# Kernel optimization log

Measured on AMD Instinct MI355X. Metric: run time of the kernel, lower is better.

The kernel has to match this reference:

```python
import jax, jax.numpy as jnp
import numpy as np

S, A, B, D = 4, 64, 2048, 384
H1, H2, H3 = 128, 128, 64


def setup_inputs() -> dict:
    key = jax.random.key(0)
    ks = jax.random.split(key, 6)
    x = jax.random.normal(ks[0], (B, A, D), dtype=jnp.float32)
    species = jax.random.randint(ks[1], (A,), 0, S, dtype=jnp.int32)
    # per-species stacked MLP weights, scaled ~1/sqrt(fan_in) like reset_parameters
    W0 = jax.random.normal(ks[2], (S, D, H1), dtype=jnp.float32) / np.sqrt(D)
    W1 = jax.random.normal(ks[3], (S, H1, H2), dtype=jnp.float32) / np.sqrt(H1)
    W2 = jax.random.normal(ks[4], (S, H2, H3), dtype=jnp.float32) / np.sqrt(H2)
    W3 = jax.random.normal(ks[5], (S, H3, 1), dtype=jnp.float32) / np.sqrt(H3)
    b0 = jnp.zeros((S, H1), jnp.float32)
    b1 = jnp.zeros((S, H2), jnp.float32)
    b2 = jnp.zeros((S, H3), jnp.float32)
    b3 = jnp.zeros((S, 1), jnp.float32)
    return {"x": x, "species": species, "W0": W0, "b0": b0, "W1": W1,
            "b1": b1, "W2": W2, "b2": b2, "W3": W3, "b3": b3}


def reference(x, species, W0, b0, W1, b1, W2, b2, W3, b3):
    # Gather per-atom species weights once, then batched per-atom GEMMs.
    # x: [B, A, D]; species: [A]
    y = jnp.einsum('bad,adh->bah', x, W0[species]) + b0[species]
    y = jnp.exp(-y * y)
    y = jnp.einsum('bah,ahk->bak', y, W1[species]) + b1[species]
    y = jnp.exp(-y * y)
    y = jnp.einsum('bak,akm->bam', y, W2[species]) + b2[species]
    y = jnp.exp(-y * y)
    y = jnp.einsum('bam,amo->bao', y, W3[species]) + b3[species]  # [B, A, 1]
    return jnp.squeeze(jnp.sum(y, axis=1))  # [B]
```

## Files before the change

kernel.cpp:

```cpp
#include <hip/hip_runtime.h>

#define S_DIM 4
#define A_DIM 64
#define B_DIM 2048
#define D_DIM 384
#define H1D 128
#define H2D 128
#define H3D 64
#define MT 64

typedef __attribute__((ext_vector_type(8))) short short8;
typedef __attribute__((ext_vector_type(4))) float float4v;

__device__ __forceinline__ unsigned short f2bf(float f) {
  unsigned u = __float_as_uint(f);
  u += 0x7FFFu + ((u >> 16) & 1u);
  return (unsigned short)(u >> 16);
}

__device__ __forceinline__ void store_bf4(unsigned short* p, float4v v) {
  union { unsigned short s[4]; uint2 u; } t;
  t.s[0] = f2bf(v[0]); t.s[1] = f2bf(v[1]);
  t.s[2] = f2bf(v[2]); t.s[3] = f2bf(v[3]);
  *(uint2*)p = t.u;
}

__global__ __launch_bounds__(256) void prep_weights(
    const float* __restrict__ W0, const float* __restrict__ W1,
    const float* __restrict__ W2,
    unsigned short* __restrict__ W0T, unsigned short* __restrict__ W1T,
    unsigned short* __restrict__ W2T) {
  __shared__ float tile[32][33];
  int b = blockIdx.x;
  const float* src; unsigned short* dst; int R, C, dt, ht, s;
  if (b < 192) {
    s = b / 48; int t = b % 48; dt = t / 4; ht = t % 4;
    src = W0 + s * D_DIM * H1D; dst = W0T + s * H1D * D_DIM; R = D_DIM; C = H1D;
  } else if (b < 256) {
    int bb = b - 192; s = bb / 16; int t = bb % 16; dt = t / 4; ht = t % 4;
    src = W1 + s * H1D * H2D; dst = W1T + s * H2D * H1D; R = H1D; C = H2D;
  } else {
    int bb = b - 256; s = bb / 8; int t = bb % 8; dt = t / 2; ht = t % 2;
    src = W2 + s * H2D * H3D; dst = W2T + s * H3D * H2D; R = H2D; C = H3D;
  }
  int tx = threadIdx.x & 31, ty = threadIdx.x >> 5;
#pragma unroll
  for (int k = 0; k < 4; ++k)
    tile[ty + 8 * k][tx] = src[(size_t)(dt * 32 + ty + 8 * k) * C + ht * 32 + tx];
  __syncthreads();
#pragma unroll
  for (int k = 0; k < 4; ++k)
    dst[(size_t)(ht * 32 + ty + 8 * k) * R + dt * 32 + tx] = f2bf(tile[tx][ty + 8 * k]);
}

__global__ __launch_bounds__(256, 4) void mlp_fused(
    const float* __restrict__ x, const int* __restrict__ species,
    const unsigned short* __restrict__ W0T, const unsigned short* __restrict__ W1T,
    const unsigned short* __restrict__ W2T,
    const float* __restrict__ b0, const float* __restrict__ b1,
    const float* __restrict__ b2, const float* __restrict__ W3,
    const float* __restrict__ b3, float* __restrict__ out) {
  __shared__ __align__(16) unsigned short xbuf0[MT * 136];
  __shared__ __align__(16) unsigned short xbuf1[MT * 136];
  __shared__ float W3s[H3D];
  unsigned short* H0 = xbuf1;
  unsigned short* H1 = xbuf0;
  float* H2 = (float*)xbuf1;

  const int a = blockIdx.y;
  const int brow0 = blockIdx.x * MT;
  const int sp = species[a];
  const int tid = threadIdx.x;
  const int wave = tid >> 6;
  const int lane = tid & 63;
  const int q = lane >> 4;
  const int r = lane & 15;

  const float4v zero = {0.f, 0.f, 0.f, 0.f};

  const int srow = tid >> 2;
  const int c4 = tid & 3;
  const float* xrow = x + ((size_t)(brow0 + srow) * A_DIM + a) * D_DIM + c4 * 4;
  const unsigned short* w0base =
      W0T + (size_t)sp * H1D * D_DIM + (wave * 32 + r) * D_DIM + q * 8;

  float4v xv[8];
#pragma unroll
  for (int j = 0; j < 8; ++j) xv[j] = *(const float4v*)(xrow + j * 16);
  if (tid < H3D) W3s[tid] = W3[sp * H3D + tid];
  short8 bf[4][2];
#pragma unroll
  for (int kk = 0; kk < 4; ++kk)
#pragma unroll
    for (int n = 0; n < 2; ++n)
      bf[kk][n] = *(const short8*)(w0base + n * 16 * D_DIM + kk * 32);
  {
    unsigned short* xd = xbuf0 + srow * 136 + c4 * 4;
#pragma unroll
    for (int j = 0; j < 8; ++j) store_bf4(xd + j * 16, xv[j]);
  }
  __syncthreads();

  float4v acc0[4][2];
#pragma unroll
  for (int g = 0; g < 4; ++g) { acc0[g][0] = zero; acc0[g][1] = zero; }

#pragma unroll
  for (int j = 0; j < 8; ++j) xv[j] = *(const float4v*)(xrow + 128 + j * 16);
#pragma unroll
  for (int g = 0; g < 4; ++g)
#pragma unroll
    for (int kk = 0; kk < 4; ++kk) {
      short8 af = *(const short8*)(xbuf0 + (g * 16 + r) * 136 + kk * 32 + q * 8);
      acc0[g][0] = __builtin_amdgcn_mfma_f32_16x16x32_bf16(af, bf[kk][0], acc0[g][0], 0, 0, 0);
      acc0[g][1] = __builtin_amdgcn_mfma_f32_16x16x32_bf16(af, bf[kk][1], acc0[g][1], 0, 0, 0);
    }
  {
    unsigned short* xd = xbuf1 + srow * 136 + c4 * 4;
#pragma unroll
    for (int j = 0; j < 8; ++j) store_bf4(xd + j * 16, xv[j]);
  }
  __syncthreads();

#pragma unroll
  for (int kk = 0; kk < 4; ++kk)
#pragma unroll
    for (int n = 0; n < 2; ++n)
      bf[kk][n] = *(const short8*)(w0base + n * 16 * D_DIM + 128 + kk * 32);
#pragma unroll
  for (int j = 0; j < 8; ++j) xv[j] = *(const float4v*)(xrow + 256 + j * 16);
#pragma unroll
  for (int g = 0; g < 4; ++g)
#pragma unroll
    for (int kk = 0; kk < 4; ++kk) {
      short8 af = *(const short8*)(xbuf1 + (g * 16 + r) * 136 + kk * 32 + q * 8);
      acc0[g][0] = __builtin_amdgcn_mfma_f32_16x16x32_bf16(af, bf[kk][0], acc0[g][0], 0, 0, 0);
      acc0[g][1] = __builtin_amdgcn_mfma_f32_16x16x32_bf16(af, bf[kk][1], acc0[g][1], 0, 0, 0);
    }
  {
    unsigned short* xd = xbuf0 + srow * 136 + c4 * 4;
#pragma unroll
    for (int j = 0; j < 8; ++j) store_bf4(xd + j * 16, xv[j]);
  }
  __syncthreads();

#pragma unroll
  for (int kk = 0; kk < 4; ++kk)
#pragma unroll
    for (int n = 0; n < 2; ++n)
      bf[kk][n] = *(const short8*)(w0base + n * 16 * D_DIM + 256 + kk * 32);
#pragma unroll
  for (int g = 0; g < 4; ++g)
#pragma unroll
    for (int kk = 0; kk < 4; ++kk) {
      short8 af = *(const short8*)(xbuf0 + (g * 16 + r) * 136 + kk * 32 + q * 8);
      acc0[g][0] = __builtin_amdgcn_mfma_f32_16x16x32_bf16(af, bf[kk][0], acc0[g][0], 0, 0, 0);
      acc0[g][1] = __builtin_amdgcn_mfma_f32_16x16x32_bf16(af, bf[kk][1], acc0[g][1], 0, 0, 0);
    }
  {
    const float* b0p = b0 + sp * H1D;
#pragma unroll
    for (int n = 0; n < 2; ++n) {
      float bias = b0p[wave * 32 + n * 16 + r];
#pragma unroll
      for (int g = 0; g < 4; ++g)
#pragma unroll
        for (int i = 0; i < 4; ++i) {
          float y = acc0[g][n][i] + bias;
          H0[(g * 16 + q * 4 + i) * 136 + wave * 32 + n * 16 + r] = f2bf(__expf(-y * y));
        }
    }
  }
  __syncthreads();

  {
    float4v acc1[4][2];
#pragma unroll
    for (int g = 0; g < 4; ++g) { acc1[g][0] = zero; acc1[g][1] = zero; }
    const unsigned short* w1base =
        W1T + (size_t)sp * H2D * H1D + (wave * 32 + r) * H1D + q * 8;
    short8 wf[4][2];
#pragma unroll
    for (int kk = 0; kk < 4; ++kk)
#pragma unroll
      for (int n = 0; n < 2; ++n)
        wf[kk][n] = *(const short8*)(w1base + n * 16 * H1D + kk * 32);
#pragma unroll
    for (int g = 0; g < 4; ++g)
#pragma unroll
      for (int kk = 0; kk < 4; ++kk) {
        short8 af = *(const short8*)(H0 + (g * 16 + r) * 136 + kk * 32 + q * 8);
        acc1[g][0] = __builtin_amdgcn_mfma_f32_16x16x32_bf16(af, wf[kk][0], acc1[g][0], 0, 0, 0);
        acc1[g][1] = __builtin_amdgcn_mfma_f32_16x16x32_bf16(af, wf[kk][1], acc1[g][1], 0, 0, 0);
      }
    const float* b1p = b1 + sp * H2D;
#pragma unroll
    for (int n = 0; n < 2; ++n) {
      float bias = b1p[wave * 32 + n * 16 + r];
#pragma unroll
      for (int g = 0; g < 4; ++g)
#pragma unroll
        for (int i = 0; i < 4; ++i) {
          float y = acc1[g][n][i] + bias;
          H1[(g * 16 + q * 4 + i) * 136 + wave * 32 + n * 16 + r] = f2bf(__expf(-y * y));
        }
    }
  }
  __syncthreads();

  {
    float4v acc2[4];
#pragma unroll
    for (int g = 0; g < 4; ++g) acc2[g] = zero;
    const unsigned short* w2base =
        W2T + (size_t)sp * H3D * H2D + (wave * 16 + r) * H2D + q * 8;
    short8 wf[4];
#pragma unroll
    for (int kk = 0; kk < 4; ++kk)
      wf[kk] = *(const short8*)(w2base + kk * 32);
#pragma unroll
    for (int g = 0; g < 4; ++g)
#pragma unroll
      for (int kk = 0; kk < 4; ++kk) {
        short8 af = *(const short8*)(H1 + (g * 16 + r) * 136 + kk * 32 + q * 8);
        acc2[g] = __builtin_amdgcn_mfma_f32_16x16x32_bf16(af, wf[kk], acc2[g], 0, 0, 0);
      }
    float bias = b2[sp * H3D + wave * 16 + r];
#pragma unroll
    for (int g = 0; g < 4; ++g)
#pragma unroll
      for (int i = 0; i < 4; ++i) {
        float y = acc2[g][i] + bias;
        H2[(g * 16 + q * 4 + i) * 68 + wave * 16 + r] = __expf(-y * y);
      }
  }
  __syncthreads();

  {
    const int row = tid >> 2;
    const int seg = tid & 3;
    const float4v* h2p = (const float4v*)(H2 + row * 68 + seg * 16);
    const float4v* w3p = (const float4v*)(W3s + seg * 16);
    float4v sv = zero;
#pragma unroll
    for (int jj = 0; jj < 4; ++jj) sv += h2p[jj] * w3p[jj];
    float s = sv[0] + sv[1] + sv[2] + sv[3];
    s += __shfl_xor(s, 1);
    s += __shfl_xor(s, 2);
    if (seg == 0) atomicAdd(&out[brow0 + row], s + b3[sp]);
  }
}

extern "C" void kernel_launch(void* const* d_in, const int* in_sizes, int n_in,
                              void* d_out, int out_size, void* d_ws, size_t ws_size,
                              hipStream_t stream) {
  const float* x       = (const float*)d_in[0];
  const int*   species = (const int*)d_in[1];
  const float* W0 = (const float*)d_in[2];
  const float* b0 = (const float*)d_in[3];
  const float* W1 = (const float*)d_in[4];
  const float* b1 = (const float*)d_in[5];
  const float* W2 = (const float*)d_in[6];
  const float* b2 = (const float*)d_in[7];
  const float* W3 = (const float*)d_in[8];
  const float* b3 = (const float*)d_in[9];
  float* out = (float*)d_out;

  unsigned short* W0T = (unsigned short*)d_ws;
  unsigned short* W1T = W0T + S_DIM * H1D * D_DIM;
  unsigned short* W2T = W1T + S_DIM * H2D * H1D;

  hipMemsetAsync(d_out, 0, out_size * sizeof(float), stream);
  prep_weights<<<dim3(288), dim3(256), 0, stream>>>(W0, W1, W2, W0T, W1T, W2T);
  mlp_fused<<<dim3(B_DIM / MT, A_DIM), dim3(256), 0, stream>>>(
      x, species, W0T, W1T, W2T, b0, b1, b2, W3, b3, out);
}
```

Before: 310.3 us.

## Swap grid axes and coalesce x loads across 16 lanes per row

Swaps the grid so adjacent blocks handle adjacent atoms of the same batch rows, which makes consecutive blocks touch contiguous regions of x. Each row's 128-float chunk is now loaded by 16 threads with consecutive float4s, instead of 4 threads with strided float4s, for fuller memory coalescing. The LDS store pattern is remapped to match. Both changes target the global-load efficiency of the large x tensor.

```diff
diff --git a/kernel.cpp b/kernel.cpp
--- a/kernel.cpp
+++ b/kernel.cpp
@@ -8,6 +8,7 @@
 #define H2D 128
 #define H3D 64
 #define MT 64
+#define XROW (A_DIM * D_DIM)
 
 typedef __attribute__((ext_vector_type(8))) short short8;
 typedef __attribute__((ext_vector_type(4))) float float4v;
@@ -67,8 +68,8 @@
   unsigned short* H1 = xbuf0;
   float* H2 = (float*)xbuf1;
 
-  const int a = blockIdx.y;
-  const int brow0 = blockIdx.x * MT;
+  const int a = blockIdx.x;
+  const int brow0 = blockIdx.y * MT;
   const int sp = species[a];
   const int tid = threadIdx.x;
   const int wave = tid >> 6;
@@ -78,15 +79,20 @@
 
   const float4v zero = {0.f, 0.f, 0.f, 0.f};
 
-  const int srow = tid >> 2;
-  const int c4 = tid & 3;
-  const float* xrow = x + ((size_t)(brow0 + srow) * A_DIM + a) * D_DIM + c4 * 4;
+  const int srow16 = tid >> 4;
+  const int c16 = tid & 15;
+  const float* xbase = x + ((size_t)(brow0 + srow16) * A_DIM + a) * D_DIM + c16 * 4;
+  unsigned short* xd0 = xbuf0 + srow16 * 136 + c16 * 4;
+  unsigned short* xd1 = xbuf1 + srow16 * 136 + c16 * 4;
   const unsigned short* w0base =
       W0T + (size_t)sp * H1D * D_DIM + (wave * 32 + r) * D_DIM + q * 8;
 
   float4v xv[8];
 #pragma unroll
-  for (int j = 0; j < 8; ++j) xv[j] = *(const float4v*)(xrow + j * 16);
+  for (int h = 0; h < 4; ++h) {
+    xv[2 * h]     = *(const float4v*)(xbase + (size_t)h * 16 * XROW);
+    xv[2 * h + 1] = *(const float4v*)(xbase + (size_t)h * 16 * XROW + 64);
+  }
   if (tid < H3D) W3s[tid] = W3[sp * H3D + tid];
   short8 bf[4][2];
 #pragma unroll
@@ -94,10 +100,10 @@
 #pragma unroll
     for (int n = 0; n < 2; ++n)
       bf[kk][n] = *(const short8*)(w0base + n * 16 * D_DIM + kk * 32);
-  {
-    unsigned short* xd = xbuf0 + srow * 136 + c4 * 4;
-#pragma unroll
-    for (int j = 0; j < 8; ++j) store_bf4(xd + j * 16, xv[j]);
+#pragma unroll
+  for (int h = 0; h < 4; ++h) {
+    store_bf4(xd0 + h * 16 * 136, xv[2 * h]);
+    store_bf4(xd0 + h * 16 * 136 + 64, xv[2 * h + 1]);
   }
   __syncthreads();
 
@@ -106,7 +112,10 @@
   for (int g = 0; g < 4; ++g) { acc0[g][0] = zero; acc0[g][1] = zero; }
 
 #pragma unroll
-  for (int j = 0; j < 8; ++j) xv[j] = *(const float4v*)(xrow + 128 + j * 16);
+  for (int h = 0; h < 4; ++h) {
+    xv[2 * h]     = *(const float4v*)(xbase + (size_t)h * 16 * XROW + 128);
+    xv[2 * h + 1] = *(const float4v*)(xbase + (size_t)h * 16 * XROW + 192);
+  }
 #pragma unroll
   for (int g = 0; g < 4; ++g)
 #pragma unroll
@@ -115,10 +124,10 @@
       acc0[g][0] = __builtin_amdgcn_mfma_f32_16x16x32_bf16(af, bf[kk][0], acc0[g][0], 0, 0, 0);
       acc0[g][1] = __builtin_amdgcn_mfma_f32_16x16x32_bf16(af, bf[kk][1], acc0[g][1], 0, 0, 0);
     }
-  {
-    unsigned short* xd = xbuf1 + srow * 136 + c4 * 4;
-#pragma unroll
-    for (int j = 0; j < 8; ++j) store_bf4(xd + j * 16, xv[j]);
+#pragma unroll
+  for (int h = 0; h < 4; ++h) {
+    store_bf4(xd1 + h * 16 * 136, xv[2 * h]);
+    store_bf4(xd1 + h * 16 * 136 + 64, xv[2 * h + 1]);
   }
   __syncthreads();
 
@@ -128,7 +137,10 @@
     for (int n = 0; n < 2; ++n)
       bf[kk][n] = *(const short8*)(w0base + n * 16 * D_DIM + 128 + kk * 32);
 #pragma unroll
-  for (int j = 0; j < 8; ++j) xv[j] = *(const float4v*)(xrow + 256 + j * 16);
+  for (int h = 0; h < 4; ++h) {
+    xv[2 * h]     = *(const float4v*)(xbase + (size_t)h * 16 * XROW + 256);
+    xv[2 * h + 1] = *(const float4v*)(xbase + (size_t)h * 16 * XROW + 320);
+  }
 #pragma unroll
   for (int g = 0; g < 4; ++g)
 #pragma unroll
@@ -137,10 +149,10 @@
       acc0[g][0] = __builtin_amdgcn_mfma_f32_16x16x32_bf16(af, bf[kk][0], acc0[g][0], 0, 0, 0);
       acc0[g][1] = __builtin_amdgcn_mfma_f32_16x16x32_bf16(af, bf[kk][1], acc0[g][1], 0, 0, 0);
     }
-  {
-    unsigned short* xd = xbuf0 + srow * 136 + c4 * 4;
-#pragma unroll
-    for (int j = 0; j < 8; ++j) store_bf4(xd + j * 16, xv[j]);
+#pragma unroll
+  for (int h = 0; h < 4; ++h) {
+    store_bf4(xd0 + h * 16 * 136, xv[2 * h]);
+    store_bf4(xd0 + h * 16 * 136 + 64, xv[2 * h + 1]);
   }
   __syncthreads();
 
@@ -272,6 +284,6 @@
 
   hipMemsetAsync(d_out, 0, out_size * sizeof(float), stream);
   prep_weights<<<dim3(288), dim3(256), 0, stream>>>(W0, W1, W2, W0T, W1T, W2T);
-  mlp_fused<<<dim3(B_DIM / MT, A_DIM), dim3(256), 0, stream>>>(
+  mlp_fused<<<dim3(A_DIM, B_DIM / MT), dim3(256), 0, stream>>>(
       x, species, W0T, W1T, W2T, b0, b1, b2, W3, b3, out);
 }
```

Result: no change. 305.2 us (-1.6%).
